# Performance work log

Measured on AMD Instinct MI355X. Metric: run time of the kernel, lower is better.

Reference implementation:

```python
import jax, jax.numpy as jnp
import numpy as np

S, B, D, Z, C, H = 256, 1024, 64, 32, 64, 128
L = 2 * S + 3  # len(ext_ts); _xs[0::2][1:-1] must match xs -> L = 2*S+3


def setup_inputs() -> dict:
    key = jax.random.key(0)
    ks = jax.random.split(key, 16)

    def xavier(k, out_d, in_d):
        lim = float(np.sqrt(6.0 / (in_d + out_d)))
        return jax.random.uniform(k, (out_d, in_d), minval=-lim, maxval=lim, dtype=jnp.float32)

    bias = lambda n: jnp.full((n,), 0.01, jnp.float32)  # m.bias.data.fill_(0.01)

    return {
        "xs": jax.random.normal(ks[0], (S, B, D), jnp.float32),
        "ext_ts": jnp.arange(L, dtype=jnp.float32) * 0.01,  # spacing <= dt=0.02 -> 1 euler step/interval
        "eps_z0": jax.random.normal(ks[1], (B, Z), jnp.float32),
        "dW": jax.random.normal(ks[2], (L - 1, B, Z), jnp.float32),  # standard normal; scaled by sqrt(dt) inside
        "gru_Wih": xavier(ks[3], 3 * H, D),
        "gru_Whh": xavier(ks[4], 3 * H, H),
        "gru_bih": jnp.zeros((3 * H,), jnp.float32),
        "gru_bhh": jnp.zeros((3 * H,), jnp.float32),
        "enc_W": xavier(ks[5], C, H), "enc_b": bias(C),
        "qz0_W": xavier(ks[6], 2 * Z, C), "qz0_b": bias(2 * Z),
        "f_W1": xavier(ks[7], H, Z + 1), "f_b1": bias(H),
        "f_W2": xavier(ks[8], H, H), "f_b2": bias(H),
        "f_W3": xavier(ks[9], Z, H), "f_b3": bias(Z),
        "g_W1": xavier(ks[10], H, Z + 1), "g_b1": bias(H),
        "g_W2": xavier(ks[11], Z, H), "g_b2": bias(Z),
        "proj_W": xavier(ks[12], D, Z), "proj_b": bias(D),
        "pz0_mean": jnp.zeros((1, Z), jnp.float32),
        "pz0_logstd": jnp.zeros((1, Z), jnp.float32),
    }


def reference(xs, ext_ts, eps_z0, dW, gru_Wih, gru_Whh, gru_bih, gru_bhh,
              enc_W, enc_b, qz0_W, qz0_b,
              f_W1, f_b1, f_W2, f_b2, f_W3, f_b3,
              g_W1, g_b1, g_W2, g_b2,
              proj_W, proj_b, pz0_mean, pz0_logstd):
    nb = xs.shape[1]
    # ---- Encoder: GRU over time-reversed xs; only ctx[0] (after flip-back) is
    # used, which equals lin(final hidden of the reversed-sequence GRU).
    x_rev = xs[::-1]
    gi_all = jnp.einsum('sbd,hd->sbh', x_rev, gru_Wih) + gru_bih  # (S,B,3H)

    def gru_step(h, gi_t):
        gh = h @ gru_Whh.T + gru_bhh
        i_r, i_z, i_n = jnp.split(gi_t, 3, axis=-1)
        h_r, h_z, h_n = jnp.split(gh, 3, axis=-1)
        r = jax.nn.sigmoid(i_r + h_r)
        zg = jax.nn.sigmoid(i_z + h_z)
        n = jnp.tanh(i_n + r * h_n)
        return (1.0 - zg) * n + zg * h, None

    hT, _ = jax.lax.scan(gru_step, jnp.zeros((nb, gru_Whh.shape[1]), xs.dtype), gi_all)
    ctx0 = hT @ enc_W.T + enc_b

    # ---- q(z0) and reparameterized sample
    q = ctx0 @ qz0_W.T + qz0_b
    qz0_mean, qz0_logstd = jnp.split(q, 2, axis=1)
    z0 = qz0_mean + jnp.exp(qz0_logstd) * eps_z0

    # ---- Euler-Maruyama SDE integration (diagonal noise), one step per interval
    dts = ext_ts[1:] - ext_ts[:-1]

    def sde_step(z, inp):
        t, dt, dw = inp
        tcol = jnp.broadcast_to(t.reshape(1, 1), (z.shape[0], 1)).astype(z.dtype)
        tz = jnp.concatenate([tcol, z], axis=1)  # (B, Z+1)
        h1 = jax.nn.relu(tz @ f_W1.T + f_b1)
        h2 = jax.nn.relu(h1 @ f_W2.T + f_b2)
        drift = h2 @ f_W3.T + f_b3
        gh = jax.nn.relu(tz @ g_W1.T + g_b1)
        diff = gh @ g_W2.T + g_b2
        z_new = z + drift * dt + diff * (jnp.sqrt(dt) * dw)
        return z_new, z_new

    _, zs_rest = jax.lax.scan(sde_step, z0, (ext_ts[:-1], dts, dW))
    zs = jnp.concatenate([z0[None], zs_rest], axis=0)  # (L,B,Z)

    # ---- project to data space and compute losses
    xs_hat = jnp.einsum('lbz,dz->lbd', zs, proj_W) + proj_b
    recon_xs = xs_hat[0::2][1:-1]   # (S,B,D)
    interp_xs = xs_hat[1::2][1:-1]  # (S-1,B,D)
    recon_loss = jnp.mean((recon_xs - xs) ** 2)

    # KL( N(qm, e^qls) || N(pm, e^pls) ), summed over latent, averaged over batch
    kl = (pz0_logstd - qz0_logstd
          + (jnp.exp(2.0 * qz0_logstd) + (qz0_mean - pz0_mean) ** 2)
          / (2.0 * jnp.exp(2.0 * pz0_logstd)) - 0.5)
    logqp0 = jnp.mean(jnp.sum(kl, axis=1))
    return recon_loss, logqp0, interp_xs
```

## Files before the change

### kernel.cpp

```cpp
#include <hip/hip_runtime.h>

typedef _Float16 f16;
typedef _Float16 h2 __attribute__((ext_vector_type(2)));
typedef _Float16 h8 __attribute__((ext_vector_type(8)));
typedef _Float16 v8h __attribute__((ext_vector_type(8)));
typedef _Float16 v4h __attribute__((ext_vector_type(4)));
typedef float    f4 __attribute__((ext_vector_type(4)));
typedef float    v4f __attribute__((ext_vector_type(4)));
typedef float    f2 __attribute__((ext_vector_type(2)));

#define S_  256
#define B_  1024
#define D_  64
#define H_  128
#define Z_  32
#define BD_ (B_*D_)
#define NSTEP 514

__device__ __forceinline__ float fdot2(h2 a, h2 b, float c) {
#if __has_builtin(__builtin_amdgcn_fdot2)
  return __builtin_amdgcn_fdot2(a, b, c, false);
#else
  return c + (float)a[0]*(float)b[0] + (float)a[1]*(float)b[1];
#endif
}

__device__ __forceinline__ float dot8(h8 a, h8 w, float acc) {
  h2 a0 = __builtin_shufflevector(a, a, 0, 1), w0 = __builtin_shufflevector(w, w, 0, 1);
  h2 a1 = __builtin_shufflevector(a, a, 2, 3), w1 = __builtin_shufflevector(w, w, 2, 3);
  h2 a2 = __builtin_shufflevector(a, a, 4, 5), w2 = __builtin_shufflevector(w, w, 4, 5);
  h2 a3 = __builtin_shufflevector(a, a, 6, 7), w3 = __builtin_shufflevector(w, w, 6, 7);
  acc = fdot2(a0, w0, acc);
  acc = fdot2(a1, w1, acc);
  acc = fdot2(a2, w2, acc);
  acc = fdot2(a3, w3, acc);
  return acc;
}

__device__ __forceinline__ h8 ld8(const float* p) {
  f4 a = *(const f4*)p;
  f4 b = *(const f4*)(p + 4);
  h8 w;
  w[0]=(f16)a[0]; w[1]=(f16)a[1]; w[2]=(f16)a[2]; w[3]=(f16)a[3];
  w[4]=(f16)b[0]; w[5]=(f16)b[1]; w[6]=(f16)b[2]; w[7]=(f16)b[3];
  return w;
}

__device__ __forceinline__ float sigm(float x) { return 1.f / (1.f + __expf(-x)); }
__device__ __forceinline__ float tanh_(float x) {
  float e = __expf(-2.f * fabsf(x));
  float t = (1.f - e) / (1.f + e);
  return copysignf(t, x);
}

__global__ __launch_bounds__(256, 2) void gru_kernel(
    const float* __restrict__ xs, const float* __restrict__ Wih,
    const float* __restrict__ Whh, const float* __restrict__ bih,
    const float* __restrict__ bhh, float* __restrict__ hT)
{
  __shared__ h8 actH[16][2];
  __shared__ h8 xv[8][2];
  __shared__ float part[2][2][4][128];

  const int t  = threadIdx.x;
  const int b0 = blockIdx.x * 2;
  const int jh = t & 127;
  const int kh = t >> 7;

  h8 whr[8], whz[8], whn[8], wxr[4], wxz[4], wxn[4];
  {
    const float* pr = Whh + jh*H_        + kh*64;
    const float* pz = Whh + (jh+128)*H_  + kh*64;
    const float* pn = Whh + (jh+256)*H_  + kh*64;
    #pragma unroll
    for (int c = 0; c < 8; ++c) {
      whr[c] = ld8(pr + c*8);
      whz[c] = ld8(pz + c*8);
      whn[c] = ld8(pn + c*8);
    }
    const float* qr = Wih + jh*D_        + kh*32;
    const float* qz = Wih + (jh+128)*D_  + kh*32;
    const float* qn = Wih + (jh+256)*D_  + kh*32;
    #pragma unroll
    for (int c = 0; c < 4; ++c) {
      wxr[c] = ld8(qr + c*8);
      wxz[c] = ld8(qz + c*8);
      wxn[c] = ld8(qn + c*8);
    }
  }
  const int gb = t >> 7, hd = t & 127;
  const float bir = bih[hd], biz = bih[hd+128], bin = bih[hd+256];
  const float bhr = bhh[hd], bhz = bhh[hd+128], bhn = bhh[hd+256];
  float hmast = 0.f;

  if (t < 32) { h8 zz = {}; actH[t>>1][t&1] = zz; }
  if (t < 128) {
    int b = t >> 6, d = t & 63;
    float x0 = xs[(S_-1)*BD_ + (b0+b)*D_ + d];
    ((f16*)xv)[((d>>3)*2 + b)*8 + (d&7)] = (f16)x0;
  }
  __syncthreads();

  #pragma unroll 1
  for (int s = 0; s < S_; ++s) {
    float xnext = 0.f;
    if (s < S_-1 && t < 128) {
      int b = t >> 6, d = t & 63;
      xnext = xs[(S_-2-s)*BD_ + (b0+b)*D_ + d];
    }
    float pr0=0.f, pz0=0.f, pnh0=0.f, pnx0=0.f;
    float pr1=0.f, pz1=0.f, pnh1=0.f, pnx1=0.f;
    #pragma unroll
    for (int c = 0; c < 8; ++c) {
      h8 a0 = actH[kh*8 + c][0];
      h8 a1 = actH[kh*8 + c][1];
      pr0  = dot8(a0, whr[c], pr0);   pr1  = dot8(a1, whr[c], pr1);
      pz0  = dot8(a0, whz[c], pz0);   pz1  = dot8(a1, whz[c], pz1);
      pnh0 = dot8(a0, whn[c], pnh0);  pnh1 = dot8(a1, whn[c], pnh1);
    }
    #pragma unroll
    for (int c = 0; c < 4; ++c) {
      h8 a0 = xv[kh*4 + c][0];
      h8 a1 = xv[kh*4 + c][1];
      pr0  = dot8(a0, wxr[c], pr0);   pr1  = dot8(a1, wxr[c], pr1);
      pz0  = dot8(a0, wxz[c], pz0);   pz1  = dot8(a1, wxz[c], pz1);
      pnx0 = dot8(a0, wxn[c], pnx0);  pnx1 = dot8(a1, wxn[c], pnx1);
    }
    part[kh][0][0][jh] = pr0;   part[kh][1][0][jh] = pr1;
    part[kh][0][1][jh] = pz0;   part[kh][1][1][jh] = pz1;
    part[kh][0][2][jh] = pnh0;  part[kh][1][2][jh] = pnh1;
    part[kh][0][3][jh] = pnx0;  part[kh][1][3][jh] = pnx1;
    __syncthreads();

    {
      float pr  = part[0][gb][0][hd] + part[1][gb][0][hd];
      float pz  = part[0][gb][1][hd] + part[1][gb][1][hd];
      float pnh = part[0][gb][2][hd] + part[1][gb][2][hd];
      float pnx = part[0][gb][3][hd] + part[1][gb][3][hd];
      float r  = sigm(pr + bir + bhr);
      float zg = sigm(pz + biz + bhz);
      float n  = tanh_(pnx + bin + r*(pnh + bhn));
      hmast = (1.f - zg)*n + zg*hmast;
      ((f16*)actH)[((hd>>3)*2 + gb)*8 + (hd&7)] = (f16)hmast;
    }
    if (s < S_-1 && t < 128) {
      int b = t >> 6, d = t & 63;
      ((f16*)xv)[((d>>3)*2 + b)*8 + (d&7)] = (f16)xnext;
    }
    __syncthreads();
  }
  hT[(b0 + gb)*H_ + hd] = hmast;
}

__global__ __launch_bounds__(256) void enc_kernel(
    const float* __restrict__ hT, const float* __restrict__ encW,
    const float* __restrict__ encB, const float* __restrict__ qW,
    const float* __restrict__ qB, const float* __restrict__ eps,
    const float* __restrict__ pm, const float* __restrict__ pls,
    float* __restrict__ z0, float* __restrict__ out)
{
  __shared__ float hTl[4][128];
  __shared__ float ctx[4][64];
  __shared__ float ql[4][64];
  const int t = threadIdx.x;
  const int b0 = blockIdx.x * 4;
  const int lb = t >> 6, j = t & 63;

  for (int i = t; i < 512; i += 256) hTl[i>>7][i&127] = hT[b0*H_ + i];
  __syncthreads();

  float acc = encB[j];
  #pragma unroll
  for (int k = 0; k < 128; k += 4) {
    f4 w = *(const f4*)&encW[j*128 + k];
    acc += hTl[lb][k]*w[0] + hTl[lb][k+1]*w[1] + hTl[lb][k+2]*w[2] + hTl[lb][k+3]*w[3];
  }
  ctx[lb][j] = acc;
  __syncthreads();

  float q = qB[j];
  #pragma unroll
  for (int k = 0; k < 64; k += 4) {
    f4 w = *(const f4*)&qW[j*64 + k];
    q += ctx[lb][k]*w[0] + ctx[lb][k+1]*w[1] + ctx[lb][k+2]*w[2] + ctx[lb][k+3]*w[3];
  }
  ql[lb][j] = q;
  __syncthreads();

  float kl = 0.f;
  if (j < 32) {
    float mean = ql[lb][j], ls = ql[lb][j+32];
    z0[(b0+lb)*Z_ + j] = mean + __expf(ls)*eps[(b0+lb)*Z_ + j];
    float pmj = pm[j], plsj = pls[j];
    float dm = mean - pmj;
    kl = plsj - ls + (__expf(2.f*ls) + dm*dm) / (2.f*__expf(2.f*plsj)) - 0.5f;
  }
  #pragma unroll
  for (int s2 = 32; s2 > 0; s2 >>= 1) kl += __shfl_down(kl, s2, 64);
  if (j == 0) atomicAdd(out + 1, kl * (1.f/1024.f));
}

__global__ __launch_bounds__(256, 1) void sde_mfma_kernel(
    const float* __restrict__ z0, const float* __restrict__ ts,
    const float* __restrict__ dW, const float* __restrict__ xs,
    const float* __restrict__ fW1, const float* __restrict__ fb1,
    const float* __restrict__ fW2, const float* __restrict__ fb2,
    const float* __restrict__ fW3, const float* __restrict__ fb3,
    const float* __restrict__ gW1, const float* __restrict__ gb1,
    const float* __restrict__ gW2, const float* __restrict__ gb2,
    const float* __restrict__ pW, const float* __restrict__ pb,
    float* __restrict__ out)
{
  __shared__ f16 Xa[16*72];
  __shared__ f16 h1A[16*168];
  __shared__ f16 ghA[16*168];
  __shared__ f16 h2A[16*168];
  __shared__ float tsL[516];
  __shared__ float lred[4];

  const int t    = threadIdx.x;
  const int wid  = t >> 6;
  const int lane = t & 63;
  const int lr = lane & 15;
  const int lg = lane >> 4;
  const int r0 = blockIdx.x * 16;
  const int wz = wid & 1;

  v8h w1r[8];
  #pragma unroll
  for (int nl = 0; nl < 4; ++nl) {
    const int n = wid*4 + nl;
    const float* src = (n < 8) ? (fW1 + (n*16+lr)*33) : (gW1 + ((n-8)*16+lr)*33);
    const float bsv  = (n < 8) ? fb1[n*16+lr] : gb1[(n-8)*16+lr];
    #pragma unroll
    for (int ks = 0; ks < 2; ++ks) {
      v8h w;
      #pragma unroll
      for (int j = 0; j < 8; ++j) {
        const int kp = ks*32 + lg*8 + j;
        float v;
        if (kp < 32)                   v = src[1+kp];
        else if (kp == 32 || kp == 34) v = src[0];
        else if (kp == 33)             v = bsv;
        else                           v = 0.f;
        w[j] = (f16)v;
      }
      w1r[nl*2+ks] = w;
    }
  }
  v8h w2r[10];
  #pragma unroll
  for (int nl = 0; nl < 2; ++nl) {
    const int n = wid*2 + nl;
    const float* src = fW2 + (n*16+lr)*128;
    const float bsv = fb2[n*16+lr];
    #pragma unroll
    for (int ks = 0; ks < 5; ++ks) {
      v8h w;
      #pragma unroll
      for (int j = 0; j < 8; ++j) {
        const int kp = ks*32 + lg*8 + j;
        float v = (kp < 128) ? src[kp] : ((kp == 128) ? bsv : 0.f);
        w[j] = (f16)v;
      }
      w2r[nl*5+ks] = w;
    }
  }
  v8h w3d[5], w3g[5];
  {
    const float* sd = fW3 + (wz*16+lr)*128;
    const float* sg = gW2 + (wz*16+lr)*128;
    const float bd = fb3[wz*16+lr], bg = gb2[wz*16+lr];
    #pragma unroll
    for (int ks = 0; ks < 5; ++ks) {
      v8h wd, wg;
      #pragma unroll
      for (int j = 0; j < 8; ++j) {
        const int kp = ks*32 + lg*8 + j;
        wd[j] = (f16)((kp < 128) ? sd[kp] : ((kp == 128) ? bd : 0.f));
        wg[j] = (f16)((kp < 128) ? sg[kp] : ((kp == 128) ? bg : 0.f));
      }
      w3d[ks] = wd; w3g[ks] = wg;
    }
  }
  v8h pwr[2];
  {
    const float* sp = pW + (wid*16+lr)*32;
    const float bp = pb[wid*16+lr];
    #pragma unroll
    for (int ks = 0; ks < 2; ++ks) {
      v8h w;
      #pragma unroll
      for (int j = 0; j < 8; ++j) {
        const int kp = ks*32 + lg*8 + j;
        w[j] = (f16)((kp < 32) ? sp[kp] : ((kp == 33) ? bp : 0.f));
      }
      pwr[ks] = w;
    }
  }

  for (int i = t; i < 16*72; i += 256) Xa[i] = (f16)0.f;
  for (int i = t; i < 16*168; i += 256) {
    h1A[i] = (f16)0.f; ghA[i] = (f16)0.f; h2A[i] = (f16)0.f;
  }
  for (int i = t; i < 515; i += 256) tsL[i] = ts[i];
  __syncthreads();
  if (t < 16) {
    Xa[t*72 + 33] = (f16)1.f;
    h1A[t*168 + 128] = (f16)1.f;
    ghA[t*168 + 128] = (f16)1.f;
    h2A[t*168 + 128] = (f16)1.f;
    const float t0 = tsL[0];
    const f16 th = (f16)t0;
    Xa[t*72 + 32] = th;
    Xa[t*72 + 34] = (f16)(t0 - (float)th);
  }
  const v4f zero4 = {0.f, 0.f, 0.f, 0.f};
  v4f zm = zero4;
  if (wid < 2) {
    zm = *(const v4f*)&z0[(r0+lr)*Z_ + wid*16 + lg*4];
    v4h a;
    #pragma unroll
    for (int i = 0; i < 4; ++i) a[i] = (f16)zm[i];
    *(v4h*)&Xa[lr*72 + wid*16 + lg*4] = a;
  }
  float loss = 0.f;
  __syncthreads();

  #pragma unroll 1
  for (int l = 0; l < NSTEP; ++l) {
    const float dt  = tsL[l+1] - tsL[l];
    const float sdt = sqrtf(dt);
    const int ln = l + 1;
    const bool ev = ((ln & 1) == 0) && ln >= 2 && ln <= 512;
    const bool od = ((ln & 1) == 1) && ln >= 3 && ln <= 511;

    v4f dwv = zero4;
    if (wid < 2) dwv = *(const v4f*)&dW[(l*B_ + r0 + lr)*Z_ + wid*16 + lg*4];
    v4f xv = zero4;
    if (ev) xv = *(const v4f*)&xs[(((ln-2)>>1)*B_ + r0 + lr)*D_ + wid*16 + lg*4];

    {
      const v8h bx0 = *(const v8h*)&Xa[lr*72 +  0 + lg*8];
      const v8h bx1 = *(const v8h*)&Xa[lr*72 + 32 + lg*8];
      #pragma unroll
      for (int nl = 0; nl < 4; ++nl) {
        v4f acc = __builtin_amdgcn_mfma_f32_16x16x32_f16(w1r[nl*2+0], bx0, zero4, 0, 0, 0);
        acc = __builtin_amdgcn_mfma_f32_16x16x32_f16(w1r[nl*2+1], bx1, acc, 0, 0, 0);
        v4h o;
        #pragma unroll
        for (int i = 0; i < 4; ++i) o[i] = (f16)fmaxf(acc[i], 0.f);
        if (wid < 2) *(v4h*)&h1A[lr*168 + (wid*4+nl)*16 + lg*4] = o;
        else         *(v4h*)&ghA[lr*168 + ((wid-2)*4+nl)*16 + lg*4] = o;
      }
    }
    __syncthreads();

    {
      v8h bh[5];
      #pragma unroll
      for (int ks = 0; ks < 5; ++ks) bh[ks] = *(const v8h*)&h1A[lr*168 + ks*32 + lg*8];
      #pragma unroll
      for (int nl = 0; nl < 2; ++nl) {
        v4f acc = zero4;
        #pragma unroll
        for (int ks = 0; ks < 5; ++ks)
          acc = __builtin_amdgcn_mfma_f32_16x16x32_f16(w2r[nl*5+ks], bh[ks], acc, 0, 0, 0);
        v4h o;
        #pragma unroll
        for (int i = 0; i < 4; ++i) o[i] = (f16)fmaxf(acc[i], 0.f);
        *(v4h*)&h2A[lr*168 + (wid*2+nl)*16 + lg*4] = o;
      }
    }
    __syncthreads();

    if (wid < 2) {
      v4f dac = zero4, fac = zero4;
      #pragma unroll
      for (int ks = 0; ks < 5; ++ks) {
        const v8h b2f = *(const v8h*)&h2A[lr*168 + ks*32 + lg*8];
        const v8h bgf = *(const v8h*)&ghA[lr*168 + ks*32 + lg*8];
        dac = __builtin_amdgcn_mfma_f32_16x16x32_f16(w3d[ks], b2f, dac, 0, 0, 0);
        fac = __builtin_amdgcn_mfma_f32_16x16x32_f16(w3g[ks], bgf, fac, 0, 0, 0);
      }
      #pragma unroll
      for (int i = 0; i < 4; ++i) zm[i] += dac[i]*dt + fac[i]*(sdt*dwv[i]);
      v4h a;
      #pragma unroll
      for (int i = 0; i < 4; ++i) a[i] = (f16)zm[i];
      *(v4h*)&Xa[lr*72 + wid*16 + lg*4] = a;
    } else if (wid == 3 && lg == 0) {
      const float tn = tsL[l+1];
      const f16 th = (f16)tn;
      Xa[lr*72 + 32] = th;
      Xa[lr*72 + 34] = (f16)(tn - (float)th);
    }
    __syncthreads();

    if (ev || od) {
      const v8h px0 = *(const v8h*)&Xa[lr*72 +  0 + lg*8];
      const v8h px1 = *(const v8h*)&Xa[lr*72 + 32 + lg*8];
      v4f a = __builtin_amdgcn_mfma_f32_16x16x32_f16(pwr[0], px0, zero4, 0, 0, 0);
      v4f p = __builtin_amdgcn_mfma_f32_16x16x32_f16(pwr[1], px1, a, 0, 0, 0);
      if (ev) {
        #pragma unroll
        for (int i = 0; i < 4; ++i) { float d = p[i] - xv[i]; loss = fmaf(d, d, loss); }
      } else {
        float* op = out + 2 + (((ln-3)>>1)*B_ + r0 + lr)*D_ + wid*16 + lg*4;
        *(f2*)&op[0] = (f2){p[0], p[1]};
        *(f2*)&op[2] = (f2){p[2], p[3]};
      }
    }
  }

  #pragma unroll
  for (int s2 = 32; s2 > 0; s2 >>= 1) loss += __shfl_down(loss, s2, 64);
  if (lane == 0) lred[wid] = loss;
  __syncthreads();
  if (t == 0)
    atomicAdd(out + 0, (lred[0] + lred[1] + lred[2] + lred[3]) * (1.f/16777216.f));
}

extern "C" void kernel_launch(void* const* d_in, const int* in_sizes, int n_in,
                              void* d_out, int out_size, void* d_ws, size_t ws_size,
                              hipStream_t stream) {
  (void)in_sizes; (void)n_in; (void)out_size; (void)ws_size;
  const float* xs   = (const float*)d_in[0];
  const float* ts   = (const float*)d_in[1];
  const float* eps  = (const float*)d_in[2];
  const float* dWp  = (const float*)d_in[3];
  const float* Wih  = (const float*)d_in[4];
  const float* Whh  = (const float*)d_in[5];
  const float* bih  = (const float*)d_in[6];
  const float* bhh  = (const float*)d_in[7];
  const float* encW = (const float*)d_in[8];
  const float* encB = (const float*)d_in[9];
  const float* qW   = (const float*)d_in[10];
  const float* qB   = (const float*)d_in[11];
  const float* fW1  = (const float*)d_in[12];
  const float* fb1  = (const float*)d_in[13];
  const float* fW2  = (const float*)d_in[14];
  const float* fb2  = (const float*)d_in[15];
  const float* fW3  = (const float*)d_in[16];
  const float* fb3  = (const float*)d_in[17];
  const float* gW1  = (const float*)d_in[18];
  const float* gb1  = (const float*)d_in[19];
  const float* gW2  = (const float*)d_in[20];
  const float* gb2  = (const float*)d_in[21];
  const float* pW   = (const float*)d_in[22];
  const float* pb   = (const float*)d_in[23];
  const float* pm   = (const float*)d_in[24];
  const float* pls  = (const float*)d_in[25];

  float* out = (float*)d_out;
  float* ws  = (float*)d_ws;
  float* hT = ws;
  float* z0 = ws + 131072;

  hipMemsetAsync(d_out, 0, 2*sizeof(float), stream);
  hipLaunchKernelGGL(gru_kernel, dim3(512), dim3(256), 0, stream,
                     xs, Wih, Whh, bih, bhh, hT);
  hipLaunchKernelGGL(enc_kernel, dim3(256), dim3(256), 0, stream,
                     hT, encW, encB, qW, qB, eps, pm, pls, z0, out);
  hipLaunchKernelGGL(sde_mfma_kernel, dim3(64), dim3(256), 0, stream,
                     z0, ts, dWp, xs, fW1, fb1, fW2, fb2, fW3, fb3,
                     gW1, gb1, gW2, gb2, pW, pb, out);
}
```

Measured before the change: 1.278 ms.

## Rewrite GRU encoder with MFMA over 16-row batch tiles and double-buffered hidden state

```diff
diff --git a/kernel.cpp b/kernel.cpp
--- a/kernel.cpp
+++ b/kernel.cpp
@@ -17,26 +17,6 @@
 #define BD_ (B_*D_)
 #define NSTEP 514
 
-__device__ __forceinline__ float fdot2(h2 a, h2 b, float c) {
-#if __has_builtin(__builtin_amdgcn_fdot2)
-  return __builtin_amdgcn_fdot2(a, b, c, false);
-#else
-  return c + (float)a[0]*(float)b[0] + (float)a[1]*(float)b[1];
-#endif
-}
-
-__device__ __forceinline__ float dot8(h8 a, h8 w, float acc) {
-  h2 a0 = __builtin_shufflevector(a, a, 0, 1), w0 = __builtin_shufflevector(w, w, 0, 1);
-  h2 a1 = __builtin_shufflevector(a, a, 2, 3), w1 = __builtin_shufflevector(w, w, 2, 3);
-  h2 a2 = __builtin_shufflevector(a, a, 4, 5), w2 = __builtin_shufflevector(w, w, 4, 5);
-  h2 a3 = __builtin_shufflevector(a, a, 6, 7), w3 = __builtin_shufflevector(w, w, 6, 7);
-  acc = fdot2(a0, w0, acc);
-  acc = fdot2(a1, w1, acc);
-  acc = fdot2(a2, w2, acc);
-  acc = fdot2(a3, w3, acc);
-  return acc;
-}
-
 __device__ __forceinline__ h8 ld8(const float* p) {
   f4 a = *(const f4*)p;
   f4 b = *(const f4*)(p + 4);
@@ -53,103 +33,106 @@
   return copysignf(t, x);
 }
 
-__global__ __launch_bounds__(256, 2) void gru_kernel(
+__global__ __launch_bounds__(256, 1) void gru_mfma_kernel(
     const float* __restrict__ xs, const float* __restrict__ Wih,
     const float* __restrict__ Whh, const float* __restrict__ bih,
     const float* __restrict__ bhh, float* __restrict__ hT)
 {
-  __shared__ h8 actH[16][2];
-  __shared__ h8 xv[8][2];
-  __shared__ float part[2][2][4][128];
-
-  const int t  = threadIdx.x;
-  const int b0 = blockIdx.x * 2;
-  const int jh = t & 127;
-  const int kh = t >> 7;
-
-  h8 whr[8], whz[8], whn[8], wxr[4], wxz[4], wxn[4];
-  {
-    const float* pr = Whh + jh*H_        + kh*64;
-    const float* pz = Whh + (jh+128)*H_  + kh*64;
-    const float* pn = Whh + (jh+256)*H_  + kh*64;
-    #pragma unroll
-    for (int c = 0; c < 8; ++c) {
-      whr[c] = ld8(pr + c*8);
-      whz[c] = ld8(pz + c*8);
-      whn[c] = ld8(pn + c*8);
-    }
-    const float* qr = Wih + jh*D_        + kh*32;
-    const float* qz = Wih + (jh+128)*D_  + kh*32;
-    const float* qn = Wih + (jh+256)*D_  + kh*32;
-    #pragma unroll
-    for (int c = 0; c < 4; ++c) {
-      wxr[c] = ld8(qr + c*8);
-      wxz[c] = ld8(qz + c*8);
-      wxn[c] = ld8(qn + c*8);
-    }
-  }
-  const int gb = t >> 7, hd = t & 127;
-  const float bir = bih[hd], biz = bih[hd+128], bin = bih[hd+256];
-  const float bhr = bhh[hd], bhz = bhh[hd+128], bhn = bhh[hd+256];
-  float hmast = 0.f;
-
-  if (t < 32) { h8 zz = {}; actH[t>>1][t&1] = zz; }
-  if (t < 128) {
-    int b = t >> 6, d = t & 63;
-    float x0 = xs[(S_-1)*BD_ + (b0+b)*D_ + d];
-    ((f16*)xv)[((d>>3)*2 + b)*8 + (d&7)] = (f16)x0;
-  }
-  __syncthreads();
-
+  __shared__ f16 hB[2][16][136];
+
+  const int t    = threadIdx.x;
+  const int wid  = t >> 6;
+  const int lane = t & 63;
+  const int lr = lane & 15;
+  const int lg = lane >> 4;
+  const int r0 = blockIdx.x * 16;
+
+  v8h whhR[2][4], whhZ[2][4], whhN[2][4];
+  v8h wihR[2][2], wihZ[2][2], wihN[2][2];
+  #pragma unroll
+  for (int tt = 0; tt < 2; ++tt) {
+    const int nr = wid*32 + tt*16 + lr;
+    #pragma unroll
+    for (int ks = 0; ks < 4; ++ks) {
+      whhR[tt][ks] = ld8(Whh + (      nr)*H_ + ks*32 + lg*8);
+      whhZ[tt][ks] = ld8(Whh + (128 + nr)*H_ + ks*32 + lg*8);
+      whhN[tt][ks] = ld8(Whh + (256 + nr)*H_ + ks*32 + lg*8);
+    }
+    #pragma unroll
+    for (int ks = 0; ks < 2; ++ks) {
+      wihR[tt][ks] = ld8(Wih + (      nr)*D_ + ks*32 + lg*8);
+      wihZ[tt][ks] = ld8(Wih + (128 + nr)*D_ + ks*32 + lg*8);
+      wihN[tt][ks] = ld8(Wih + (256 + nr)*D_ + ks*32 + lg*8);
+    }
+  }
+  v4f birh[2], bizh[2], binv[2], bhnv[2];
+  #pragma unroll
+  for (int tt = 0; tt < 2; ++tt) {
+    const int nb = wid*32 + tt*16 + lg*4;
+    v4f a = *(const v4f*)&bih[nb],     b = *(const v4f*)&bhh[nb];
+    v4f c = *(const v4f*)&bih[128+nb], d = *(const v4f*)&bhh[128+nb];
+    birh[tt] = a + b;
+    bizh[tt] = c + d;
+    binv[tt] = *(const v4f*)&bih[256+nb];
+    bhnv[tt] = *(const v4f*)&bhh[256+nb];
+  }
+
+  for (int i = t; i < 16*136; i += 256) ((f16*)hB[0])[i] = (f16)0.f;
+  v4f hm[2] = { {0.f,0.f,0.f,0.f}, {0.f,0.f,0.f,0.f} };
+  const v4f zero4 = {0.f, 0.f, 0.f, 0.f};
+
+  v8h bx0 = ld8(xs + (S_-1)*BD_ + (r0+lr)*D_ + lg*8);
+  v8h bx1 = ld8(xs + (S_-1)*BD_ + (r0+lr)*D_ + 32 + lg*8);
+  __syncthreads();
+
+  int p = 0;
   #pragma unroll 1
   for (int s = 0; s < S_; ++s) {
-    float xnext = 0.f;
-    if (s < S_-1 && t < 128) {
-      int b = t >> 6, d = t & 63;
-      xnext = xs[(S_-2-s)*BD_ + (b0+b)*D_ + d];
-    }
-    float pr0=0.f, pz0=0.f, pnh0=0.f, pnx0=0.f;
-    float pr1=0.f, pz1=0.f, pnh1=0.f, pnx1=0.f;
-    #pragma unroll
-    for (int c = 0; c < 8; ++c) {
-      h8 a0 = actH[kh*8 + c][0];
-      h8 a1 = actH[kh*8 + c][1];
-      pr0  = dot8(a0, whr[c], pr0);   pr1  = dot8(a1, whr[c], pr1);
-      pz0  = dot8(a0, whz[c], pz0);   pz1  = dot8(a1, whz[c], pz1);
-      pnh0 = dot8(a0, whn[c], pnh0);  pnh1 = dot8(a1, whn[c], pnh1);
-    }
-    #pragma unroll
-    for (int c = 0; c < 4; ++c) {
-      h8 a0 = xv[kh*4 + c][0];
-      h8 a1 = xv[kh*4 + c][1];
-      pr0  = dot8(a0, wxr[c], pr0);   pr1  = dot8(a1, wxr[c], pr1);
-      pz0  = dot8(a0, wxz[c], pz0);   pz1  = dot8(a1, wxz[c], pz1);
-      pnx0 = dot8(a0, wxn[c], pnx0);  pnx1 = dot8(a1, wxn[c], pnx1);
-    }
-    part[kh][0][0][jh] = pr0;   part[kh][1][0][jh] = pr1;
-    part[kh][0][1][jh] = pz0;   part[kh][1][1][jh] = pz1;
-    part[kh][0][2][jh] = pnh0;  part[kh][1][2][jh] = pnh1;
-    part[kh][0][3][jh] = pnx0;  part[kh][1][3][jh] = pnx1;
+    v8h nx0 = bx0, nx1 = bx1;
+    if (s < S_-1) {
+      const float* xp = xs + (S_-2-s)*BD_ + (r0+lr)*D_;
+      nx0 = ld8(xp + lg*8);
+      nx1 = ld8(xp + 32 + lg*8);
+    }
+    v8h bh[4];
+    #pragma unroll
+    for (int ks = 0; ks < 4; ++ks)
+      bh[ks] = *(const v8h*)&hB[p][lr][ks*32 + lg*8];
+
+    #pragma unroll
+    for (int tt = 0; tt < 2; ++tt) {
+      v4f ar  = __builtin_amdgcn_mfma_f32_16x16x32_f16(wihR[tt][0], bx0, zero4, 0,0,0);
+      v4f az  = __builtin_amdgcn_mfma_f32_16x16x32_f16(wihZ[tt][0], bx0, zero4, 0,0,0);
+      v4f anx = __builtin_amdgcn_mfma_f32_16x16x32_f16(wihN[tt][0], bx0, zero4, 0,0,0);
+      ar  = __builtin_amdgcn_mfma_f32_16x16x32_f16(wihR[tt][1], bx1, ar,  0,0,0);
+      az  = __builtin_amdgcn_mfma_f32_16x16x32_f16(wihZ[tt][1], bx1, az,  0,0,0);
+      anx = __builtin_amdgcn_mfma_f32_16x16x32_f16(wihN[tt][1], bx1, anx, 0,0,0);
+      v4f anh = zero4;
+      #pragma unroll
+      for (int ks = 0; ks < 4; ++ks) {
+        ar  = __builtin_amdgcn_mfma_f32_16x16x32_f16(whhR[tt][ks], bh[ks], ar,  0,0,0);
+        az  = __builtin_amdgcn_mfma_f32_16x16x32_f16(whhZ[tt][ks], bh[ks], az,  0,0,0);
+        anh = __builtin_amdgcn_mfma_f32_16x16x32_f16(whhN[tt][ks], bh[ks], anh, 0,0,0);
+      }
+      v4h o;
+      #pragma unroll
+      for (int i = 0; i < 4; ++i) {
+        float r  = sigm(ar[i] + birh[tt][i]);
+        float zg = sigm(az[i] + bizh[tt][i]);
+        float n  = tanh_(anx[i] + binv[tt][i] + r*(anh[i] + bhnv[tt][i]));
+        hm[tt][i] = (1.f - zg)*n + zg*hm[tt][i];
+        o[i] = (f16)hm[tt][i];
+      }
+      *(v4h*)&hB[p^1][lr][wid*32 + tt*16 + lg*4] = o;
+    }
     __syncthreads();
-
-    {
-      float pr  = part[0][gb][0][hd] + part[1][gb][0][hd];
-      float pz  = part[0][gb][1][hd] + part[1][gb][1][hd];
-      float pnh = part[0][gb][2][hd] + part[1][gb][2][hd];
-      float pnx = part[0][gb][3][hd] + part[1][gb][3][hd];
-      float r  = sigm(pr + bir + bhr);
-      float zg = sigm(pz + biz + bhz);
-      float n  = tanh_(pnx + bin + r*(pnh + bhn));
-      hmast = (1.f - zg)*n + zg*hmast;
-      ((f16*)actH)[((hd>>3)*2 + gb)*8 + (hd&7)] = (f16)hmast;
-    }
-    if (s < S_-1 && t < 128) {
-      int b = t >> 6, d = t & 63;
-      ((f16*)xv)[((d>>3)*2 + b)*8 + (d&7)] = (f16)xnext;
-    }
-    __syncthreads();
-  }
-  hT[(b0 + gb)*H_ + hd] = hmast;
+    p ^= 1;
+    bx0 = nx0; bx1 = nx1;
+  }
+
+  #pragma unroll
+  for (int tt = 0; tt < 2; ++tt)
+    *(v4f*)&hT[(r0+lr)*H_ + wid*32 + tt*16 + lg*4] = hm[tt];
 }
 
 __global__ __launch_bounds__(256) void enc_kernel(
@@ -458,7 +441,7 @@
   float* z0 = ws + 131072;
 
   hipMemsetAsync(d_out, 0, 2*sizeof(float), stream);
-  hipLaunchKernelGGL(gru_kernel, dim3(512), dim3(256), 0, stream,
+  hipLaunchKernelGGL(gru_mfma_kernel, dim3(64), dim3(256), 0, stream,
                      xs, Wih, Whh, bih, bhh, hT);
   hipLaunchKernelGGL(enc_kernel, dim3(256), dim3(256), 0, stream,
                      hT, encW, encB, qW, qB, eps, pm, pls, z0, out);
```

Measured after the change: 1.270 ms. No clear change (-0.6%).
